# Kernel optimization log

Hardware: AMD Instinct MI355X
Metric: run time of the kernel (lower is better)

## Reference

```python
import jax, jax.numpy as jnp
import numpy as np

N, L, D = 8, 256, 256  # batch, length, hidden
DP = D + 1             # flag=True appends bias column


def setup_inputs() -> dict:
    key = jax.random.key(0)
    ks = jax.random.split(key, 7)
    s = 0.02  # xavier-like init scale
    return {
        "layer1": jax.random.normal(ks[0], (N, L, D), jnp.float32),
        "layer2": jax.random.normal(ks[1], (N, L, D), jnp.float32),
        "h1": jax.random.normal(ks[2], (N, L, D), jnp.float32),
        "h2": jax.random.normal(ks[3], (N, L, D), jnp.float32),
        "W_1": jax.random.normal(ks[4], (DP, DP, D), jnp.float32) * s,
        "W_2": jax.random.normal(ks[5], (DP, DP, D), jnp.float32) * s,
        "W_3": jax.random.normal(ks[6], (D, D), jnp.float32) * s,
    }


def reference(layer1, layer2, h1, h2, W_1, W_2, W_3):
    n, l, _ = layer1.shape
    ones = jnp.ones((n, l, 1), layer1.dtype)
    l1 = jnp.concatenate([layer1, ones], axis=-1)  # [n, L, D+1]
    l2 = jnp.concatenate([layer2, ones], axis=-1)  # [n, L, D+1]
    # factorized triaffine: two nijc intermediates, then rank contraction
    layer_l = jnp.einsum('nia,abc,njb,nic->nijc', l1, W_1, l2, h1, optimize='optimal')
    layer_r = jnp.einsum('nia,abc,njb,nic->nijc', l1, W_2, l2, h2, optimize='optimal')
    return jnp.einsum('nijc,cd,nijd->nij', layer_l, W_3, layer_r, optimize='optimal')
```

## Files before the change

kernel.cpp:

```cpp
#include <hip/hip_runtime.h>

typedef __attribute__((ext_vector_type(4))) float f32x4;
typedef __attribute__((ext_vector_type(8))) short s16x8;

#define MTOTW 65792

__device__ __forceinline__ short f2bf(float f) {
    unsigned u = __builtin_bit_cast(unsigned, f);
    u = (u + 0x7fffu + ((u >> 16) & 1u)) >> 16;
    return (short)u;
}

__device__ __forceinline__ void gl16(const void* g, void* l) {
    __builtin_amdgcn_global_load_lds(
        (const __attribute__((address_space(1))) unsigned int*)g,
        (__attribute__((address_space(3))) unsigned int*)l, 16, 0, 0);
}

__global__ __launch_bounds__(256) void conv_bf16(
    const float* __restrict__ a, const float* __restrict__ b,
    short* __restrict__ ao, short* __restrict__ bo)
{
    int i = blockIdx.x * 256 + threadIdx.x;
    const int HALF = 131072;
    float4 v; short* dst;
    if (i < HALF) { v = ((const float4*)a)[i]; dst = ao + (size_t)i * 4; }
    else          { v = ((const float4*)b)[i - HALF]; dst = bo + (size_t)(i - HALF) * 4; }
    short4 o; o.x = f2bf(v.x); o.y = f2bf(v.y); o.z = f2bf(v.z); o.w = f2bf(v.w);
    *(short4*)dst = o;
}

__global__ __launch_bounds__(256) void prep_w3t(
    const float* __restrict__ W3, short* __restrict__ W3t)
{
    __shared__ float ld[32][33];
    int t = threadIdx.x, bx = blockIdx.x;
    int c0 = (bx >> 3) * 32, d0 = (bx & 7) * 32;
    int cr = t >> 3, dq = t & 7;
    float4 v = *(const float4*)&W3[(size_t)(c0 + cr) * 256 + d0 + dq * 4];
    ld[cr][dq*4+0] = v.x; ld[cr][dq*4+1] = v.y; ld[cr][dq*4+2] = v.z; ld[cr][dq*4+3] = v.w;
    __syncthreads();
    int dr = t >> 3, cq = t & 7;
    short4 o;
    o.x = f2bf(ld[cq*4+0][dr]); o.y = f2bf(ld[cq*4+1][dr]);
    o.z = f2bf(ld[cq*4+2][dr]); o.w = f2bf(ld[cq*4+3][dr]);
    *(short4*)&W3t[(size_t)(d0 + dr) * 256 + c0 + cq * 4] = o;
}

__global__ __launch_bounds__(256) void prep_wtail(
    const float* __restrict__ W1, const float* __restrict__ W2,
    short* __restrict__ Wtp1, short* __restrict__ Wtp2)
{
    __shared__ float ld[32][33];
    int t = threadIdx.x, bx = blockIdx.x;
    const float* W = blockIdx.y ? W2 : W1;
    short* Wtp = blockIdx.y ? Wtp2 : Wtp1;
    int a0 = (bx >> 3) * 32, c0 = (bx & 7) * 32;
    int ar = t >> 3, cq = t & 7;
    float4 v = *(const float4*)&W[(size_t)(a0 + ar) * MTOTW + 65536 + c0 + cq * 4];
    ld[ar][cq*4+0] = v.x; ld[ar][cq*4+1] = v.y; ld[ar][cq*4+2] = v.z; ld[ar][cq*4+3] = v.w;
    __syncthreads();
    int cr = t >> 3, aq = t & 7;
    short4 o;
    o.x = f2bf(ld[aq*4+0][cr]); o.y = f2bf(ld[aq*4+1][cr]);
    o.z = f2bf(ld[aq*4+2][cr]); o.w = f2bf(ld[aq*4+3][cr]);
    *(short4*)&Wtp[(size_t)(c0 + cr) * 256 + a0 + aq * 4] = o;
}

__global__ __launch_bounds__(256) void prep_wp(
    const float* __restrict__ W1, const float* __restrict__ W2,
    short* __restrict__ Wp1, short* __restrict__ Wp2)
{
    __shared__ float ld[32][33];
    int t = threadIdx.x, bx = blockIdx.x;
    int b = blockIdx.y;
    const float* W = blockIdx.z ? W2 : W1;
    short* Wp = blockIdx.z ? Wp2 : Wp1;
    int a0 = (bx >> 3) * 32, c0 = (bx & 7) * 32;
    int ar = t >> 3, cq = t & 7;
    float4 v = *(const float4*)&W[(size_t)(a0 + ar) * MTOTW + (size_t)b * 256 + c0 + cq * 4];
    ld[ar][cq*4+0] = v.x; ld[ar][cq*4+1] = v.y; ld[ar][cq*4+2] = v.z; ld[ar][cq*4+3] = v.w;
    __syncthreads();
    int cr = t >> 3, aq = t & 7;
    short4 o;
    o.x = f2bf(ld[aq*4+0][cr]); o.y = f2bf(ld[aq*4+1][cr]);
    o.z = f2bf(ld[aq*4+2][cr]); o.w = f2bf(ld[aq*4+3][cr]);
    *(short4*)&Wp[((size_t)(c0 + cr) * 256 + b) * 256 + a0 + aq * 4] = o;
}

__global__ __launch_bounds__(256, 2) void tail_mfma(
    const short* __restrict__ l1b,
    const short* __restrict__ Wtp1, const short* __restrict__ Wtp2,
    const float* __restrict__ W1, const float* __restrict__ W2,
    float* __restrict__ tail1, float* __restrict__ tail2)
{
    __shared__ __align__(16) short Al[128 * 32];
    __shared__ __align__(16) short Bl[128 * 32];
    int t = threadIdx.x, w = t >> 6, lane = t & 63;
    int l4 = lane >> 2, kq = lane & 3;
    int rt = blockIdx.x, nt = blockIdx.y, ten = blockIdx.z;
    const short* Wtp = ten ? Wtp2 : Wtp1;
    const float* Wf = ten ? W2 : W1;
    float* tail = ten ? tail2 : tail1;
    const short* Ab = l1b + (size_t)(rt * 128) * 256;
    const short* Bb = Wtp + (size_t)(nt * 128) * 256;

    f32x4 acc[4][4] = {};
    int m0w = (w >> 1) * 64, n0w = (w & 1) * 64;

    for (int k0 = 0; k0 < 256; k0 += 32) {
        __syncthreads();
        #pragma unroll
        for (int q = 0; q < 4; ++q) {
            int seg = w * 4 + q;
            if (seg < 8)
                gl16(Ab + (size_t)(seg * 16 + l4) * 256 + k0 + kq * 8, &Al[seg * 512]);
            else
                gl16(Bb + (size_t)((seg - 8) * 16 + l4) * 256 + k0 + kq * 8, &Bl[(seg - 8) * 512]);
        }
        __syncthreads();
        s16x8 af[4], bf[4];
        #pragma unroll
        for (int i = 0; i < 4; ++i) {
            af[i] = *(const s16x8*)&Al[(m0w + i * 16 + (lane & 15)) * 32 + (lane >> 4) * 8];
            bf[i] = *(const s16x8*)&Bl[(n0w + i * 16 + (lane & 15)) * 32 + (lane >> 4) * 8];
        }
        #pragma unroll
        for (int mi = 0; mi < 4; ++mi)
            #pragma unroll
            for (int ni = 0; ni < 4; ++ni)
                acc[mi][ni] = __builtin_amdgcn_mfma_f32_16x16x32_bf16(af[mi], bf[ni], acc[mi][ni], 0, 0, 0);
    }
    #pragma unroll
    for (int ni = 0; ni < 4; ++ni) {
        int c = nt * 128 + n0w + ni * 16 + (lane & 15);
        float tl = Wf[(size_t)256 * MTOTW + 65536 + c];
        #pragma unroll
        for (int mi = 0; mi < 4; ++mi) {
            int r = rt * 128 + m0w + mi * 16 + (lane >> 4) * 4;
            #pragma unroll
            for (int reg = 0; reg < 4; ++reg)
                tail[(size_t)(r + reg) * 256 + c] = acc[mi][ni][reg] + tl;
        }
    }
}

__global__ __launch_bounds__(256, 2) void stage1(
    const short* __restrict__ l1b,
    const short* __restrict__ Wp1, const short* __restrict__ Wp2,
    const float* __restrict__ W1, const float* __restrict__ W2,
    short* __restrict__ T1, short* __restrict__ T2, int row0)
{
    __shared__ __align__(16) short Al[128 * 32];
    __shared__ __align__(16) short Bl[128 * 32];
    __shared__ __align__(16) short Cep[4 * 4096];
    int t = threadIdx.x, w = t >> 6, lane = t & 63;
    int l4 = lane >> 2, kq = lane & 3;

    unsigned gdx = gridDim.x;
    unsigned orig = blockIdx.x + gdx * (blockIdx.y + 2u * blockIdx.z);
    unsigned nwg = gdx * 1024u;
    unsigned swz = (orig & 7u) * (nwg >> 3) + (orig >> 3);
    int rt = swz & (gdx - 1u);
    unsigned rest = swz / gdx;
    int bt = rest & 1, zc = rest >> 1;

    int c = zc >> 1, ten = zc & 1;
    const short* Wp = ten ? Wp2 : Wp1;
    const float* Wf = ten ? W2 : W1;
    short* T = ten ? T2 : T1;
    int r0g = row0 + rt * 128;
    int b0 = bt * 128;
    const short* Ab = l1b + (size_t)r0g * 256;
    const short* Bb = Wp + ((size_t)c * 256 + b0) * 256;

    f32x4 acc[4][4] = {};
    int m0w = (w >> 1) * 64, n0w = (w & 1) * 64;

    for (int k0 = 0; k0 < 256; k0 += 32) {
        __syncthreads();
        #pragma unroll
        for (int q = 0; q < 4; ++q) {
            int seg = w * 4 + q;
            if (seg < 8)
                gl16(Ab + (size_t)(seg * 16 + l4) * 256 + k0 + kq * 8, &Al[seg * 512]);
            else
                gl16(Bb + (size_t)((seg - 8) * 16 + l4) * 256 + k0 + kq * 8, &Bl[(seg - 8) * 512]);
        }
        __syncthreads();
        s16x8 af[4], bf[4];
        #pragma unroll
        for (int i = 0; i < 4; ++i) {
            af[i] = *(const s16x8*)&Al[(m0w + i * 16 + (lane & 15)) * 32 + (lane >> 4) * 8];
            bf[i] = *(const s16x8*)&Bl[(n0w + i * 16 + (lane & 15)) * 32 + (lane >> 4) * 8];
        }
        #pragma unroll
        for (int mi = 0; mi < 4; ++mi)
            #pragma unroll
            for (int ni = 0; ni < 4; ++ni)
                acc[mi][ni] = __builtin_amdgcn_mfma_f32_16x16x32_bf16(af[mi], bf[ni], acc[mi][ni], 0, 0, 0);
    }

    short* Cw = &Cep[w * 4096];
    #pragma unroll
    for (int ni = 0; ni < 4; ++ni) {
        int b = b0 + n0w + ni * 16 + (lane & 15);
        float tl = Wf[(size_t)256 * MTOTW + (size_t)b * 256 + c];
        #pragma unroll
        for (int mi = 0; mi < 4; ++mi)
            #pragma unroll
            for (int reg = 0; reg < 4; ++reg) {
                int lr = mi * 16 + (lane >> 4) * 4 + reg;
                int lc = ni * 16 + (lane & 15);
                Cw[lr * 64 + lc] = f2bf(acc[mi][ni][reg] + tl);
            }
    }
    #pragma unroll
    for (int s = 0; s < 8; ++s) {
        int row = s * 8 + (lane >> 3);
        int co = (lane & 7) * 8;
        int rl = rt * 128 + m0w + row;
        int gb = b0 + n0w + co;
        *(int4*)&T[((size_t)rl * 256 + c) * 256 + gb] = *(int4*)&Cw[row * 64 + co];
    }
}

__global__ __launch_bounds__(256, 2) void stage2(
    const short* __restrict__ l2b,
    const short* __restrict__ T1, const short* __restrict__ T2,
    const float* __restrict__ tail1, const float* __restrict__ tail2,
    const float* __restrict__ h1, const float* __restrict__ h2,
    const short* __restrict__ W3t, float* __restrict__ out, int row0)
{
    __shared__ __align__(16) short Al[64 * 32];
    __shared__ __align__(16) short B1l[256 * 32];
    __shared__ __align__(16) short B2l[256 * 32];
    __shared__ __align__(16) short V1[64 * 264];
    __shared__ float part[64 * 4];
    int t = threadIdx.x, w = t >> 6, lane = t & 63;
    int l4 = lane >> 2, kq = lane & 3;

    unsigned orig = blockIdx.x + (blockIdx.y << 2);
    unsigned nwg = gridDim.y << 2;
    unsigned swz = (orig & 7u) * (nwg >> 3) + (orig >> 3);
    int jt = swz & 3, rl = swz >> 2;

    int rg = row0 + rl, n = rg >> 8, j0 = jt * 64;
    const short* Arow = l2b + ((size_t)n * 256 + j0) * 256;
    const short* Tt1 = T1 + (size_t)rl * 65536;
    const short* Tt2 = T2 + (size_t)rl * 65536;
    int n0w = w * 64;

    f32x4 acc1[4][4] = {}, acc2[4][4] = {};
    for (int k0 = 0; k0 < 256; k0 += 32) {
        __syncthreads();
        #pragma unroll
        for (int q = 0; q < 9; ++q) {
            int seg = w * 9 + q;
            const short* gb; short* lb;
            if (seg < 4)       { gb = Arow + (size_t)(seg * 16 + l4) * 256;        lb = &Al[seg * 512]; }
            else if (seg < 20) { int s = seg - 4;  gb = Tt1 + (size_t)(s * 16 + l4) * 256; lb = &B1l[s * 512]; }
            else               { int s = seg - 20; gb = Tt2 + (size_t)(s * 16 + l4) * 256; lb = &B2l[s * 512]; }
            gl16(gb + k0 + kq * 8, lb);
        }
        __syncthreads();
        s16x8 af[4], b1[4], b2[4];
        #pragma unroll
        for (int i = 0; i < 4; ++i) {
            af[i] = *(const s16x8*)&Al[(i * 16 + (lane & 15)) * 32 + (lane >> 4) * 8];
            b1[i] = *(const s16x8*)&B1l[(n0w + i * 16 + (lane & 15)) * 32 + (lane >> 4) * 8];
            b2[i] = *(const s16x8*)&B2l[(n0w + i * 16 + (lane & 15)) * 32 + (lane >> 4) * 8];
        }
        #pragma unroll
        for (int mi = 0; mi < 4; ++mi)
            #pragma unroll
            for (int ni = 0; ni < 4; ++ni) {
                acc1[mi][ni] = __builtin_amdgcn_mfma_f32_16x16x32_bf16(af[mi], b1[ni], acc1[mi][ni], 0, 0, 0);
                acc2[mi][ni] = __builtin_amdgcn_mfma_f32_16x16x32_bf16(af[mi], b2[ni], acc2[mi][ni], 0, 0, 0);
            }
    }

    f32x4 v2[4][4];
    #pragma unroll
    for (int ni = 0; ni < 4; ++ni) {
        int c = n0w + ni * 16 + (lane & 15);
        float hh1 = h1[(size_t)rg * 256 + c], tl1 = tail1[(size_t)rg * 256 + c];
        float hh2 = h2[(size_t)rg * 256 + c], tl2 = tail2[(size_t)rg * 256 + c];
        #pragma unroll
        for (int mi = 0; mi < 4; ++mi)
            #pragma unroll
            for (int reg = 0; reg < 4; ++reg) {
                int j = mi * 16 + (lane >> 4) * 4 + reg;
                V1[j * 264 + c] = f2bf(hh1 * (acc1[mi][ni][reg] + tl1));
                v2[mi][ni][reg] = hh2 * (acc2[mi][ni][reg] + tl2);
            }
    }

    f32x4 accP[4][4] = {};
    for (int k0 = 0; k0 < 256; k0 += 32) {
        __syncthreads();
        #pragma unroll
        for (int q = 0; q < 4; ++q) {
            int s = w * 4 + q;
            gl16(W3t + (size_t)(s * 16 + l4) * 256 + k0 + kq * 8, &B1l[s * 512]);
        }
        __syncthreads();
        s16x8 af[4], bf[4];
        #pragma unroll
        for (int i = 0; i < 4; ++i) {
            af[i] = *(const s16x8*)&V1[(i * 16 + (lane & 15)) * 264 + k0 + (lane >> 4) * 8];
            bf[i] = *(const s16x8*)&B1l[(n0w + i * 16 + (lane & 15)) * 32 + (lane >> 4) * 8];
        }
        #pragma unroll
        for (int mi = 0; mi < 4; ++mi)
            #pragma unroll
            for (int ni = 0; ni < 4; ++ni)
                accP[mi][ni] = __builtin_amdgcn_mfma_f32_16x16x32_bf16(af[mi], bf[ni], accP[mi][ni], 0, 0, 0);
    }

    #pragma unroll
    for (int mi = 0; mi < 4; ++mi)
        #pragma unroll
        for (int reg = 0; reg < 4; ++reg) {
            float s = 0.f;
            #pragma unroll
            for (int ni = 0; ni < 4; ++ni) s += accP[mi][ni][reg] * v2[mi][ni][reg];
            s += __shfl_xor(s, 1); s += __shfl_xor(s, 2);
            s += __shfl_xor(s, 4); s += __shfl_xor(s, 8);
            if ((lane & 15) == 0)
                part[(mi * 16 + (lane >> 4) * 4 + reg) * 4 + w] = s;
        }
    __syncthreads();
    if (t < 64)
        out[(size_t)rg * 256 + j0 + t] = part[t*4] + part[t*4+1] + part[t*4+2] + part[t*4+3];
}

extern "C" void kernel_launch(void* const* d_in, const int* in_sizes, int n_in,
                              void* d_out, int out_size, void* d_ws, size_t ws_size,
                              hipStream_t stream) {
    const float* layer1 = (const float*)d_in[0];
    const float* layer2 = (const float*)d_in[1];
    const float* h1     = (const float*)d_in[2];
    const float* h2     = (const float*)d_in[3];
    const float* W1     = (const float*)d_in[4];
    const float* W2     = (const float*)d_in[5];
    const float* W3     = (const float*)d_in[6];
    float* out = (float*)d_out;

    short* Wp1  = (short*)d_ws;
    short* Wp2  = Wp1 + 16777216;
    short* l1b  = Wp2 + 16777216;
    short* l2b  = l1b + 524288;
    short* W3t  = l2b + 524288;
    short* Wtp1 = W3t + 65536;
    short* Wtp2 = Wtp1 + 65536;
    float* tail1 = (float*)(Wtp2 + 65536);
    float* tail2 = tail1 + 524288;
    short* T1   = (short*)(tail2 + 524288);
    const size_t head = (size_t)(16777216*2 + 524288*2 + 65536*3) * 2 + (size_t)524288 * 2 * 4;
    int chunk = 2048;
    while (head + (size_t)chunk * 262144 > ws_size && chunk > 128) chunk >>= 1;
    short* T2 = T1 + (size_t)chunk * 65536;

    conv_bf16<<<1024, 256, 0, stream>>>(layer1, layer2, l1b, l2b);
    prep_w3t<<<64, 256, 0, stream>>>(W3, W3t);
    prep_wtail<<<dim3(64, 2), 256, 0, stream>>>(W1, W2, Wtp1, Wtp2);
    prep_wp<<<dim3(64, 256, 2), 256, 0, stream>>>(W1, W2, Wp1, Wp2);
    tail_mfma<<<dim3(16, 2, 2), 256, 0, stream>>>(l1b, Wtp1, Wtp2, W1, W2, tail1, tail2);

    for (int row0 = 0; row0 < 2048; row0 += chunk) {
        stage1<<<dim3(chunk / 128, 2, 512), 256, 0, stream>>>(
            l1b, Wp1, Wp2, W1, W2, T1, T2, row0);
        stage2<<<dim3(4, chunk), 256, 0, stream>>>(
            l2b, T1, T2, tail1, tail2, h1, h2, W3t, out, row0);
    }
}
```

Measured before the change: 750.9 us.

## Double-buffer LDS tiles in stage1 and stage2 GEMM loops

```diff
diff --git a/kernel.cpp b/kernel.cpp
--- a/kernel.cpp
+++ b/kernel.cpp
@@ -151,9 +151,7 @@
     const float* __restrict__ W1, const float* __restrict__ W2,
     short* __restrict__ T1, short* __restrict__ T2, int row0)
 {
-    __shared__ __align__(16) short Al[128 * 32];
-    __shared__ __align__(16) short Bl[128 * 32];
-    __shared__ __align__(16) short Cep[4 * 4096];
+    __shared__ __align__(16) short S[16384];
     int t = threadIdx.x, w = t >> 6, lane = t & 63;
     int l4 = lane >> 2, kq = lane & 3;
 
@@ -177,31 +175,44 @@
     f32x4 acc[4][4] = {};
     int m0w = (w >> 1) * 64, n0w = (w & 1) * 64;
 
-    for (int k0 = 0; k0 < 256; k0 += 32) {
-        __syncthreads();
-        #pragma unroll
-        for (int q = 0; q < 4; ++q) {
-            int seg = w * 4 + q;
-            if (seg < 8)
-                gl16(Ab + (size_t)(seg * 16 + l4) * 256 + k0 + kq * 8, &Al[seg * 512]);
-            else
-                gl16(Bb + (size_t)((seg - 8) * 16 + l4) * 256 + k0 + kq * 8, &Bl[(seg - 8) * 512]);
-        }
-        __syncthreads();
+    #pragma unroll
+    for (int q = 0; q < 4; ++q) {
+        int seg = w * 4 + q;
+        if (seg < 8)
+            gl16(Ab + (size_t)(seg * 16 + l4) * 256 + kq * 8, &S[seg * 512]);
+        else
+            gl16(Bb + (size_t)((seg - 8) * 16 + l4) * 256 + kq * 8, &S[4096 + (seg - 8) * 512]);
+    }
+    __syncthreads();
+
+    for (int kt = 0; kt < 8; ++kt) {
+        int cur = (kt & 1) * 8192;
+        if (kt < 7) {
+            int nb = cur ^ 8192, k0 = (kt + 1) * 32;
+            #pragma unroll
+            for (int q = 0; q < 4; ++q) {
+                int seg = w * 4 + q;
+                if (seg < 8)
+                    gl16(Ab + (size_t)(seg * 16 + l4) * 256 + k0 + kq * 8, &S[nb + seg * 512]);
+                else
+                    gl16(Bb + (size_t)((seg - 8) * 16 + l4) * 256 + k0 + kq * 8, &S[nb + 4096 + (seg - 8) * 512]);
+            }
+        }
         s16x8 af[4], bf[4];
         #pragma unroll
         for (int i = 0; i < 4; ++i) {
-            af[i] = *(const s16x8*)&Al[(m0w + i * 16 + (lane & 15)) * 32 + (lane >> 4) * 8];
-            bf[i] = *(const s16x8*)&Bl[(n0w + i * 16 + (lane & 15)) * 32 + (lane >> 4) * 8];
+            af[i] = *(const s16x8*)&S[cur + (m0w + i * 16 + (lane & 15)) * 32 + (lane >> 4) * 8];
+            bf[i] = *(const s16x8*)&S[cur + 4096 + (n0w + i * 16 + (lane & 15)) * 32 + (lane >> 4) * 8];
         }
         #pragma unroll
         for (int mi = 0; mi < 4; ++mi)
             #pragma unroll
             for (int ni = 0; ni < 4; ++ni)
                 acc[mi][ni] = __builtin_amdgcn_mfma_f32_16x16x32_bf16(af[mi], bf[ni], acc[mi][ni], 0, 0, 0);
-    }
-
-    short* Cw = &Cep[w * 4096];
+        __syncthreads();
+    }
+
+    short* Cw = &S[w * 4096];
     #pragma unroll
     for (int ni = 0; ni < 4; ++ni) {
         int b = b0 + n0w + ni * 16 + (lane & 15);
@@ -232,11 +243,7 @@
     const float* __restrict__ h1, const float* __restrict__ h2,
     const short* __restrict__ W3t, float* __restrict__ out, int row0)
 {
-    __shared__ __align__(16) short Al[64 * 32];
-    __shared__ __align__(16) short B1l[256 * 32];
-    __shared__ __align__(16) short B2l[256 * 32];
-    __shared__ __align__(16) short V1[64 * 264];
-    __shared__ float part[64 * 4];
+    __shared__ __align__(16) short S2[36864];
     int t = threadIdx.x, w = t >> 6, lane = t & 63;
     int l4 = lane >> 2, kq = lane & 3;
 
@@ -252,24 +259,38 @@
     int n0w = w * 64;
 
     f32x4 acc1[4][4] = {}, acc2[4][4] = {};
-    for (int k0 = 0; k0 < 256; k0 += 32) {
-        __syncthreads();
-        #pragma unroll
-        for (int q = 0; q < 9; ++q) {
-            int seg = w * 9 + q;
-            const short* gb; short* lb;
-            if (seg < 4)       { gb = Arow + (size_t)(seg * 16 + l4) * 256;        lb = &Al[seg * 512]; }
-            else if (seg < 20) { int s = seg - 4;  gb = Tt1 + (size_t)(s * 16 + l4) * 256; lb = &B1l[s * 512]; }
-            else               { int s = seg - 20; gb = Tt2 + (size_t)(s * 16 + l4) * 256; lb = &B2l[s * 512]; }
-            gl16(gb + k0 + kq * 8, lb);
-        }
-        __syncthreads();
+
+    #pragma unroll
+    for (int q = 0; q < 9; ++q) {
+        int seg = w * 9 + q;
+        const short* gb; short* lb;
+        if (seg < 4)       { gb = Arow + (size_t)(seg * 16 + l4) * 256;        lb = &S2[seg * 512]; }
+        else if (seg < 20) { int s = seg - 4;  gb = Tt1 + (size_t)(s * 16 + l4) * 256; lb = &S2[2048 + s * 512]; }
+        else               { int s = seg - 20; gb = Tt2 + (size_t)(s * 16 + l4) * 256; lb = &S2[10240 + s * 512]; }
+        gl16(gb + kq * 8, lb);
+    }
+    __syncthreads();
+
+    for (int kt = 0; kt < 8; ++kt) {
+        int cur = (kt & 1) * 18432;
+        if (kt < 7) {
+            int nb = cur ^ 18432, k0 = (kt + 1) * 32;
+            #pragma unroll
+            for (int q = 0; q < 9; ++q) {
+                int seg = w * 9 + q;
+                const short* gb; short* lb;
+                if (seg < 4)       { gb = Arow + (size_t)(seg * 16 + l4) * 256;        lb = &S2[nb + seg * 512]; }
+                else if (seg < 20) { int s = seg - 4;  gb = Tt1 + (size_t)(s * 16 + l4) * 256; lb = &S2[nb + 2048 + s * 512]; }
+                else               { int s = seg - 20; gb = Tt2 + (size_t)(s * 16 + l4) * 256; lb = &S2[nb + 10240 + s * 512]; }
+                gl16(gb + k0 + kq * 8, lb);
+            }
+        }
         s16x8 af[4], b1[4], b2[4];
         #pragma unroll
         for (int i = 0; i < 4; ++i) {
-            af[i] = *(const s16x8*)&Al[(i * 16 + (lane & 15)) * 32 + (lane >> 4) * 8];
-            b1[i] = *(const s16x8*)&B1l[(n0w + i * 16 + (lane & 15)) * 32 + (lane >> 4) * 8];
-            b2[i] = *(const s16x8*)&B2l[(n0w + i * 16 + (lane & 15)) * 32 + (lane >> 4) * 8];
+            af[i] = *(const s16x8*)&S2[cur + (i * 16 + (lane & 15)) * 32 + (lane >> 4) * 8];
+            b1[i] = *(const s16x8*)&S2[cur + 2048 + (n0w + i * 16 + (lane & 15)) * 32 + (lane >> 4) * 8];
+            b2[i] = *(const s16x8*)&S2[cur + 10240 + (n0w + i * 16 + (lane & 15)) * 32 + (lane >> 4) * 8];
         }
         #pragma unroll
         for (int mi = 0; mi < 4; ++mi)
@@ -278,8 +299,10 @@
                 acc1[mi][ni] = __builtin_amdgcn_mfma_f32_16x16x32_bf16(af[mi], b1[ni], acc1[mi][ni], 0, 0, 0);
                 acc2[mi][ni] = __builtin_amdgcn_mfma_f32_16x16x32_bf16(af[mi], b2[ni], acc2[mi][ni], 0, 0, 0);
             }
-    }
-
+        __syncthreads();
+    }
+
+    short* V1 = &S2[0];
     f32x4 v2[4][4];
     #pragma unroll
     for (int ni = 0; ni < 4; ++ni) {
@@ -297,27 +320,39 @@
     }
 
     f32x4 accP[4][4] = {};
-    for (int k0 = 0; k0 < 256; k0 += 32) {
-        __syncthreads();
-        #pragma unroll
-        for (int q = 0; q < 4; ++q) {
-            int s = w * 4 + q;
-            gl16(W3t + (size_t)(s * 16 + l4) * 256 + k0 + kq * 8, &B1l[s * 512]);
-        }
-        __syncthreads();
+    #pragma unroll
+    for (int q = 0; q < 4; ++q) {
+        int s = w * 4 + q;
+        gl16(W3t + (size_t)(s * 16 + l4) * 256 + kq * 8, &S2[18432 + s * 512]);
+    }
+    __syncthreads();
+
+    for (int kt = 0; kt < 8; ++kt) {
+        int cur = 18432 + (kt & 1) * 8192;
+        if (kt < 7) {
+            int nb = cur ^ 8192, k0 = (kt + 1) * 32;
+            #pragma unroll
+            for (int q = 0; q < 4; ++q) {
+                int s = w * 4 + q;
+                gl16(W3t + (size_t)(s * 16 + l4) * 256 + k0 + kq * 8, &S2[nb + s * 512]);
+            }
+        }
+        int k0c = kt * 32;
         s16x8 af[4], bf[4];
         #pragma unroll
         for (int i = 0; i < 4; ++i) {
-            af[i] = *(const s16x8*)&V1[(i * 16 + (lane & 15)) * 264 + k0 + (lane >> 4) * 8];
-            bf[i] = *(const s16x8*)&B1l[(n0w + i * 16 + (lane & 15)) * 32 + (lane >> 4) * 8];
+            af[i] = *(const s16x8*)&V1[(i * 16 + (lane & 15)) * 264 + k0c + (lane >> 4) * 8];
+            bf[i] = *(const s16x8*)&S2[cur + (n0w + i * 16 + (lane & 15)) * 32 + (lane >> 4) * 8];
         }
         #pragma unroll
         for (int mi = 0; mi < 4; ++mi)
             #pragma unroll
             for (int ni = 0; ni < 4; ++ni)
                 accP[mi][ni] = __builtin_amdgcn_mfma_f32_16x16x32_bf16(af[mi], bf[ni], accP[mi][ni], 0, 0, 0);
-    }
-
+        __syncthreads();
+    }
+
+    float* part = (float*)&S2[34816];
     #pragma unroll
     for (int mi = 0; mi < 4; ++mi)
         #pragma unroll
```

Measured after the change: 761.9 us. About the same (+1.5%).

## Load MFMA operands directly from global memory instead of staging through LDS

Applied to the files above, without the earlier changes.

```diff
diff --git a/kernel.cpp b/kernel.cpp
--- a/kernel.cpp
+++ b/kernel.cpp
@@ -145,17 +145,14 @@
     }
 }
 
-__global__ __launch_bounds__(256, 2) void stage1(
+__global__ __launch_bounds__(256, 3) void stage1(
     const short* __restrict__ l1b,
     const short* __restrict__ Wp1, const short* __restrict__ Wp2,
     const float* __restrict__ W1, const float* __restrict__ W2,
     short* __restrict__ T1, short* __restrict__ T2, int row0)
 {
-    __shared__ __align__(16) short Al[128 * 32];
-    __shared__ __align__(16) short Bl[128 * 32];
     __shared__ __align__(16) short Cep[4 * 4096];
     int t = threadIdx.x, w = t >> 6, lane = t & 63;
-    int l4 = lane >> 2, kq = lane & 3;
 
     unsigned gdx = gridDim.x;
     unsigned orig = blockIdx.x + gdx * (blockIdx.y + 2u * blockIdx.z);
@@ -176,23 +173,15 @@
 
     f32x4 acc[4][4] = {};
     int m0w = (w >> 1) * 64, n0w = (w & 1) * 64;
-
+    int mrow = lane & 15, kcol = (lane >> 4) * 8;
+
+    #pragma unroll 2
     for (int k0 = 0; k0 < 256; k0 += 32) {
-        __syncthreads();
-        #pragma unroll
-        for (int q = 0; q < 4; ++q) {
-            int seg = w * 4 + q;
-            if (seg < 8)
-                gl16(Ab + (size_t)(seg * 16 + l4) * 256 + k0 + kq * 8, &Al[seg * 512]);
-            else
-                gl16(Bb + (size_t)((seg - 8) * 16 + l4) * 256 + k0 + kq * 8, &Bl[(seg - 8) * 512]);
-        }
-        __syncthreads();
         s16x8 af[4], bf[4];
         #pragma unroll
         for (int i = 0; i < 4; ++i) {
-            af[i] = *(const s16x8*)&Al[(m0w + i * 16 + (lane & 15)) * 32 + (lane >> 4) * 8];
-            bf[i] = *(const s16x8*)&Bl[(n0w + i * 16 + (lane & 15)) * 32 + (lane >> 4) * 8];
+            af[i] = *(const s16x8*)&Ab[(size_t)(m0w + i * 16 + mrow) * 256 + k0 + kcol];
+            bf[i] = *(const s16x8*)&Bb[(size_t)(n0w + i * 16 + mrow) * 256 + k0 + kcol];
         }
         #pragma unroll
         for (int mi = 0; mi < 4; ++mi)
@@ -232,13 +221,9 @@
     const float* __restrict__ h1, const float* __restrict__ h2,
     const short* __restrict__ W3t, float* __restrict__ out, int row0)
 {
-    __shared__ __align__(16) short Al[64 * 32];
-    __shared__ __align__(16) short B1l[256 * 32];
-    __shared__ __align__(16) short B2l[256 * 32];
     __shared__ __align__(16) short V1[64 * 264];
-    __shared__ float part[64 * 4];
+    __shared__ float part[256];
     int t = threadIdx.x, w = t >> 6, lane = t & 63;
-    int l4 = lane >> 2, kq = lane & 3;
 
     unsigned orig = blockIdx.x + (blockIdx.y << 2);
     unsigned nwg = gridDim.y << 2;
@@ -250,26 +235,16 @@
     const short* Tt1 = T1 + (size_t)rl * 65536;
     const short* Tt2 = T2 + (size_t)rl * 65536;
     int n0w = w * 64;
+    int mrow = lane & 15, kcol = (lane >> 4) * 8;
 
     f32x4 acc1[4][4] = {}, acc2[4][4] = {};
     for (int k0 = 0; k0 < 256; k0 += 32) {
-        __syncthreads();
-        #pragma unroll
-        for (int q = 0; q < 9; ++q) {
-            int seg = w * 9 + q;
-            const short* gb; short* lb;
-            if (seg < 4)       { gb = Arow + (size_t)(seg * 16 + l4) * 256;        lb = &Al[seg * 512]; }
-            else if (seg < 20) { int s = seg - 4;  gb = Tt1 + (size_t)(s * 16 + l4) * 256; lb = &B1l[s * 512]; }
-            else               { int s = seg - 20; gb = Tt2 + (size_t)(s * 16 + l4) * 256; lb = &B2l[s * 512]; }
-            gl16(gb + k0 + kq * 8, lb);
-        }
-        __syncthreads();
         s16x8 af[4], b1[4], b2[4];
         #pragma unroll
         for (int i = 0; i < 4; ++i) {
-            af[i] = *(const s16x8*)&Al[(i * 16 + (lane & 15)) * 32 + (lane >> 4) * 8];
-            b1[i] = *(const s16x8*)&B1l[(n0w + i * 16 + (lane & 15)) * 32 + (lane >> 4) * 8];
-            b2[i] = *(const s16x8*)&B2l[(n0w + i * 16 + (lane & 15)) * 32 + (lane >> 4) * 8];
+            af[i] = *(const s16x8*)&Arow[(size_t)(i * 16 + mrow) * 256 + k0 + kcol];
+            b1[i] = *(const s16x8*)&Tt1[(size_t)(n0w + i * 16 + mrow) * 256 + k0 + kcol];
+            b2[i] = *(const s16x8*)&Tt2[(size_t)(n0w + i * 16 + mrow) * 256 + k0 + kcol];
         }
         #pragma unroll
         for (int mi = 0; mi < 4; ++mi)
@@ -295,21 +270,15 @@
                 v2[mi][ni][reg] = hh2 * (acc2[mi][ni][reg] + tl2);
             }
     }
+    __syncthreads();
 
     f32x4 accP[4][4] = {};
     for (int k0 = 0; k0 < 256; k0 += 32) {
-        __syncthreads();
-        #pragma unroll
-        for (int q = 0; q < 4; ++q) {
-            int s = w * 4 + q;
-            gl16(W3t + (size_t)(s * 16 + l4) * 256 + k0 + kq * 8, &B1l[s * 512]);
-        }
-        __syncthreads();
         s16x8 af[4], bf[4];
         #pragma unroll
         for (int i = 0; i < 4; ++i) {
-            af[i] = *(const s16x8*)&V1[(i * 16 + (lane & 15)) * 264 + k0 + (lane >> 4) * 8];
-            bf[i] = *(const s16x8*)&B1l[(n0w + i * 16 + (lane & 15)) * 32 + (lane >> 4) * 8];
+            af[i] = *(const s16x8*)&V1[(i * 16 + mrow) * 264 + k0 + kcol];
+            bf[i] = *(const s16x8*)&W3t[(size_t)(n0w + i * 16 + mrow) * 256 + k0 + kcol];
         }
         #pragma unroll
         for (int mi = 0; mi < 4; ++mi)
```

After: 1.232 ms. +64.1%, slower.
